# Optimization experiments

Measured on AMD Instinct MI355X. Metric: run time of the kernel, lower is better.

The kernel has to match this reference:

```python
import jax, jax.numpy as jnp
import numpy as np

SEQ, BS, H, I, E = 2048, 4, 2048, 4096, 8


def setup_inputs() -> dict:
    key = jax.random.key(0)
    ks = jax.random.split(key, 5)
    s = 0.02
    return {
        "hidden_states": jax.random.normal(ks[0], (SEQ, BS, H), dtype=jnp.float32),
        "router_w": jax.random.normal(ks[1], (H, E), dtype=jnp.float32) * s,
        "gate_w": jax.random.normal(ks[2], (E, H, I), dtype=jnp.float32) * s,
        "up_w": jax.random.normal(ks[3], (E, H, I), dtype=jnp.float32) * s,
        "down_w": jax.random.normal(ks[4], (E, I, H), dtype=jnp.float32) * s,
    }


def reference(hidden_states, router_w, gate_w, up_w, down_w):
    # Router: [S,B,H] @ [H,E] -> [S,B,E]; top-1 routing (num_experts_per_tok == 1)
    router_logits = jnp.einsum("sbh,he->sbe", hidden_states, router_w)
    routing_indices = jnp.argmax(router_logits, axis=-1)  # [S,B]
    # sigmoid routing weights are computed but NOT applied in the original combine
    routing_weights = jax.nn.sigmoid(jnp.max(router_logits, axis=-1))  # noqa: F841

    out = jnp.zeros_like(hidden_states)
    for e in range(E):  # small fixed expert count
        mask = (routing_indices == e)[..., None]  # [S,B,1]
        g = jnp.einsum("sbh,hi->sbi", hidden_states, gate_w[e])
        u = jnp.einsum("sbh,hi->sbi", hidden_states, up_w[e])
        y = jnp.einsum("sbi,ih->sbh", jax.nn.silu(g) * u, down_w[e])
        out = out + jnp.where(mask, y, jnp.zeros((), out.dtype))
    return out
```

## Files before the change

kernel.cpp:

```cpp
#include <hip/hip_runtime.h>
#include <hip/hip_bf16.h>

#define T_TOKENS 8192
#define H_DIM 2048
#define I_DIM 4096
#define E_EXP 8
#define PAD_ROWS 9216

typedef __bf16 bf16x8 __attribute__((ext_vector_type(8)));
typedef float floatx4 __attribute__((ext_vector_type(4)));
typedef unsigned short ushort8 __attribute__((ext_vector_type(8)));

__device__ __forceinline__ unsigned short f2bf(float f) {
  union { float f; unsigned int i; } c; c.f = f;
  unsigned int x = c.i;
  unsigned int r = x + 0x7fffu + ((x >> 16) & 1u);
  return (unsigned short)(r >> 16);
}

__device__ __forceinline__ float bf2float(unsigned short u) {
  union { unsigned int i; float f; } c; c.i = ((unsigned int)u) << 16;
  return c.f;
}

__device__ __forceinline__ void gload_lds16(const void* g, void* l) {
  __builtin_amdgcn_global_load_lds(
      (const __attribute__((address_space(1))) void*)g,
      (__attribute__((address_space(3))) void*)l, 16, 0, 0);
}

__global__ __launch_bounds__(256) void router_kernel(const float* __restrict__ x,
                                                     const float* __restrict__ rw,
                                                     unsigned short* __restrict__ xb,
                                                     int* __restrict__ idx,
                                                     int* __restrict__ hdr) {
  const int lane = threadIdx.x & 63;
  const int t = blockIdx.x * 4 + (threadIdx.x >> 6);
  const float* xr = x + (size_t)t * H_DIM;
  unsigned short* xbr = xb + (size_t)t * H_DIM;
  float acc[8];
#pragma unroll
  for (int e = 0; e < 8; ++e) acc[e] = 0.f;
#pragma unroll
  for (int j = 0; j < 8; ++j) {
    const int c0 = (lane + j * 64) * 4;
    floatx4 v = *(const floatx4*)(xr + c0);
    ushort4 o;
    o.x = f2bf(v[0]); o.y = f2bf(v[1]); o.z = f2bf(v[2]); o.w = f2bf(v[3]);
    *(ushort4*)(xbr + c0) = o;
#pragma unroll
    for (int cc = 0; cc < 4; ++cc) {
      const float h = v[cc];
      floatx4 r0 = *(const floatx4*)(rw + (size_t)(c0 + cc) * 8);
      floatx4 r1 = *(const floatx4*)(rw + (size_t)(c0 + cc) * 8 + 4);
#pragma unroll
      for (int e = 0; e < 4; ++e) { acc[e] += h * r0[e]; acc[e + 4] += h * r1[e]; }
    }
  }
#pragma unroll
  for (int off = 32; off > 0; off >>= 1)
#pragma unroll
    for (int e = 0; e < 8; ++e) acc[e] += __shfl_xor(acc[e], off, 64);
  if (lane == 0) {
    int best = 0; float bv = acc[0];
#pragma unroll
    for (int e = 1; e < 8; ++e) if (acc[e] > bv) { bv = acc[e]; best = e; }
    idx[t] = best;
    atomicAdd(&hdr[best], 1);
  }
}

__global__ __launch_bounds__(256) void setup_kernel(int* __restrict__ hdr,
                                                    int* __restrict__ rows) {
  if (threadIdx.x == 0) {
    int b = 0;
    for (int e = 0; e < 8; ++e) {
      hdr[16 + e] = b;
      b += ((hdr[e] + 127) >> 7) << 7;
    }
  }
  for (int i = threadIdx.x; i < PAD_ROWS; i += 256) rows[i] = -1;
}

__global__ __launch_bounds__(256) void scatter_kernel(const int* __restrict__ idx,
                                                      int* __restrict__ hdr,
                                                      int* __restrict__ rows) {
  int t = blockIdx.x * 256 + threadIdx.x;
  int e = idx[t];
  int p = atomicAdd(&hdr[8 + e], 1);
  rows[hdr[16 + e] + p] = t;
}

__global__ __launch_bounds__(256) void cvt_all_kernel(const float* __restrict__ gw,
                                                      const float* __restrict__ uw,
                                                      const float* __restrict__ dw,
                                                      unsigned short* __restrict__ Wg,
                                                      unsigned short* __restrict__ Wu,
                                                      unsigned short* __restrict__ Wd) {
  int bid = blockIdx.x;
  const float* W; unsigned short* Wt; int K, N;
  if (bid < 16384) {
    W = (bid < 8192) ? gw : uw; Wt = (bid < 8192) ? Wg : Wu;
    K = H_DIM; N = I_DIM;
    bid &= 8191;
  } else {
    W = dw; Wt = Wd; K = I_DIM; N = H_DIM;
    bid -= 16384;
  }
  const int e = bid >> 10;
  const int rem = bid & 1023;
  const int nper = N >> 10;
  const int nbx = rem & (nper - 1);
  const int kg = rem / nper;
  const int nb = nbx * 1024;
  const int n0 = threadIdx.x * 4;
  const float* src = W + (size_t)e * K * N + (size_t)kg * 8 * N + nb + n0;
  unsigned short* dst = Wt + (size_t)e * K * N
                        + ((size_t)kg * (N >> 4) + (nb >> 4)) * 128;
  floatx4 a[8];
#pragma unroll
  for (int kk = 0; kk < 8; ++kk) a[kk] = *(const floatx4*)(src + (size_t)kk * N);
#pragma unroll
  for (int nn = 0; nn < 4; ++nn) {
    const int n = n0 + nn;
    ushort8 o;
#pragma unroll
    for (int kk = 0; kk < 8; ++kk) o[kk] = f2bf(a[kk][nn]);
    *(ushort8*)(dst + (size_t)(n >> 4) * 128 + (n & 15) * 8) = o;
  }
}

__global__ __launch_bounds__(256) void cvt_gu_kernel(const float* __restrict__ gw,
                                                     const float* __restrict__ uw,
                                                     unsigned short* __restrict__ Wg,
                                                     unsigned short* __restrict__ Wu) {
  const int z = blockIdx.z;
  const int e = z & 7;
  const float* W = (z < 8) ? gw : uw;
  unsigned short* Wt = (z < 8) ? Wg : Wu;
  const int kg = blockIdx.y;
  const int nb = blockIdx.x * 1024;
  const int n0 = threadIdx.x * 4;
  const float* src = W + (size_t)e * H_DIM * I_DIM + (size_t)kg * 8 * I_DIM + nb + n0;
  unsigned short* dst = Wt + (size_t)e * H_DIM * I_DIM
                        + ((size_t)kg * (I_DIM >> 4) + (nb >> 4)) * 128;
  floatx4 a[8];
#pragma unroll
  for (int kk = 0; kk < 8; ++kk) a[kk] = *(const floatx4*)(src + (size_t)kk * I_DIM);
#pragma unroll
  for (int nn = 0; nn < 4; ++nn) {
    const int n = n0 + nn;
    ushort8 o;
#pragma unroll
    for (int kk = 0; kk < 8; ++kk) o[kk] = f2bf(a[kk][nn]);
    *(ushort8*)(dst + (size_t)(n >> 4) * 128 + (n & 15) * 8) = o;
  }
}

template <int K, int N>
__global__ __launch_bounds__(256) void cvt_tile_kernel(const float* __restrict__ W,
                                                       unsigned short* __restrict__ Wt) {
  const int e = blockIdx.z;
  const int kg = blockIdx.y;
  const int nb = blockIdx.x * 1024;
  const int n0 = threadIdx.x * 4;
  const float* src = W + (size_t)e * K * N + (size_t)kg * 8 * N + nb + n0;
  unsigned short* dst = Wt + (size_t)e * K * N
                        + ((size_t)kg * (N / 16) + (nb >> 4)) * 128;
  floatx4 a[8];
#pragma unroll
  for (int kk = 0; kk < 8; ++kk) a[kk] = *(const floatx4*)(src + (size_t)kk * N);
#pragma unroll
  for (int nn = 0; nn < 4; ++nn) {
    const int n = n0 + nn;
    ushort8 o;
#pragma unroll
    for (int kk = 0; kk < 8; ++kk) o[kk] = f2bf(a[kk][nn]);
    *(ushort8*)(dst + (size_t)(n >> 4) * 128 + (n & 15) * 8) = o;
  }
}

__global__ __launch_bounds__(256, 2) void moe_gemm_gu(
    const unsigned short* __restrict__ A,
    const unsigned short* __restrict__ Bg,
    const unsigned short* __restrict__ Bu,
    const int* __restrict__ hdr,
    const int* __restrict__ rows,
    unsigned short* __restrict__ inter) {
  const int e = blockIdx.z;
  const int cnt = hdr[e];
  if ((int)blockIdx.y * 128 >= cnt) return;
  const int seg = hdr[16 + e];

  const int tid = threadIdx.x;
  const int lane = tid & 63;
  const int wv = tid >> 6;
  const int wm = (wv & 1) * 64;
  const int wn = (wv >> 1) * 64;
  const int q = lane >> 4;
  const int l15 = lane & 15;

  __shared__ unsigned short sA[128 * 64];
  __shared__ unsigned short sBg[64 * 128];
  __shared__ unsigned short sBu[64 * 128];

  const int lr = lane >> 3;
  const int colsw = (lane & 7) ^ lr;
  const unsigned short* aptr[4];
#pragma unroll
  for (int j = 0; j < 4; ++j) {
    const int R = j * 32 + wv * 8 + lr;
    int ar = rows[seg + blockIdx.y * 128 + R];
    if (ar < 0) ar = 0;
    aptr[j] = A + (size_t)ar * H_DIM + colsw * 8;
  }

  const int N16 = I_DIM / 16;
  const int ng0 = blockIdx.x * 8;
  const unsigned short* BgE = Bg + (size_t)e * I_DIM * H_DIM;
  const unsigned short* BuE = Bu + (size_t)e * I_DIM * H_DIM;

  floatx4 accg[4][4], accu[4][4];
#pragma unroll
  for (int a = 0; a < 4; ++a)
#pragma unroll
    for (int b = 0; b < 4; ++b) {
      accg[a][b] = (floatx4){0.f, 0.f, 0.f, 0.f};
      accu[a][b] = (floatx4){0.f, 0.f, 0.f, 0.f};
    }

  const int ubB = q * 1024 + l15 * 8;
  const int wn16o = (wn >> 4) * 128;

  for (int kt = 0; kt < H_DIM; kt += 64) {
#pragma unroll
    for (int j = 0; j < 4; ++j) {
      gload_lds16(aptr[j] + kt, sA + (j * 32 + wv * 8) * 64);
      const int g = j * 4 + wv;
      const int kgg = (kt >> 3) + (g >> 1);
      const size_t so = (size_t)(kgg * N16 + ng0 + (g & 1) * 4) * 128 + lane * 8;
      gload_lds16(BgE + so, sBg + g * 512);
      gload_lds16(BuE + so, sBu + g * 512);
    }
    __syncthreads();
#pragma unroll
    for (int ks = 0; ks < 64; ks += 32) {
      const int sbase = ks >> 3;
      const int bbase = ks * 128 + wn16o + ubB;
      bf16x8 af[4], bfr[4];
#pragma unroll
      for (int fm = 0; fm < 4; ++fm) {
        const int ra = wm + fm * 16 + l15;
        af[fm] = __builtin_bit_cast(bf16x8,
            *(const ushort8*)(sA + ra * 64 + (((q + sbase) ^ (ra & 7)) << 3)));
      }
#pragma unroll
      for (int fn = 0; fn < 4; ++fn)
        bfr[fn] = __builtin_bit_cast(bf16x8,
            *(const ushort8*)(sBg + bbase + fn * 128));
#pragma unroll
      for (int fm = 0; fm < 4; ++fm)
#pragma unroll
        for (int fn = 0; fn < 4; ++fn)
          accg[fm][fn] = __builtin_amdgcn_mfma_f32_16x16x32_bf16(af[fm], bfr[fn],
                                                                 accg[fm][fn], 0, 0, 0);
#pragma unroll
      for (int fn = 0; fn < 4; ++fn)
        bfr[fn] = __builtin_bit_cast(bf16x8,
            *(const ushort8*)(sBu + bbase + fn * 128));
#pragma unroll
      for (int fm = 0; fm < 4; ++fm)
#pragma unroll
        for (int fn = 0; fn < 4; ++fn)
          accu[fm][fn] = __builtin_amdgcn_mfma_f32_16x16x32_bf16(af[fm], bfr[fn],
                                                                 accu[fm][fn], 0, 0, 0);
    }
    __syncthreads();
  }

#pragma unroll
  for (int fm = 0; fm < 4; ++fm)
#pragma unroll
    for (int fn = 0; fn < 4; ++fn)
#pragma unroll
      for (int rr = 0; rr < 4; ++rr) {
        const int row = wm + fm * 16 + q * 4 + rr;
        const int col = wn + fn * 16 + l15;
        const int gm = blockIdx.y * 128 + row;
        const int gn = blockIdx.x * 128 + col;
        const float g = accg[fm][fn][rr];
        const float u = accu[fm][fn][rr];
        const float s = g / (1.f + __expf(-g));
        inter[(size_t)(seg + gm) * I_DIM + gn] = f2bf(s * u);
      }
}

__global__ __launch_bounds__(256, 2) void moe_gemm_down(
    const unsigned short* __restrict__ A,
    const unsigned short* __restrict__ Bt,
    const int* __restrict__ hdr,
    const int* __restrict__ rows,
    float* __restrict__ outp) {
  const int e = blockIdx.z;
  const int cnt = hdr[e];
  if ((int)blockIdx.y * 128 >= cnt) return;
  const int seg = hdr[16 + e];

  const int tid = threadIdx.x;
  const int lane = tid & 63;
  const int wv = tid >> 6;
  const int wm = (wv & 1) * 64;
  const int wn = (wv >> 1) * 64;
  const int q = lane >> 4;
  const int l15 = lane & 15;

  __shared__ unsigned short sA[128 * 64];
  __shared__ unsigned short sB0[64 * 128];
  __shared__ unsigned short sB1[64 * 128];

  const int lr = lane >> 3;
  const int colsw = (lane & 7) ^ lr;
  const unsigned short* aptr[4];
#pragma unroll
  for (int j = 0; j < 4; ++j) {
    const int R = j * 32 + wv * 8 + lr;
    aptr[j] = A + (size_t)(seg + blockIdx.y * 128 + R) * I_DIM + colsw * 8;
  }

  const int N16 = H_DIM / 16;
  const int ng0 = blockIdx.x * 16;
  const unsigned short* Be = Bt + (size_t)e * H_DIM * I_DIM;

  floatx4 acc0[4][4], acc1[4][4];
#pragma unroll
  for (int a = 0; a < 4; ++a)
#pragma unroll
    for (int b = 0; b < 4; ++b) {
      acc0[a][b] = (floatx4){0.f, 0.f, 0.f, 0.f};
      acc1[a][b] = (floatx4){0.f, 0.f, 0.f, 0.f};
    }

  const int ubB = q * 1024 + l15 * 8;
  const int wn16o = (wn >> 4) * 128;

  for (int kt = 0; kt < I_DIM; kt += 64) {
#pragma unroll
    for (int j = 0; j < 4; ++j) {
      gload_lds16(aptr[j] + kt, sA + (j * 32 + wv * 8) * 64);
      const int g = j * 4 + wv;
      const int kgg = (kt >> 3) + (g >> 1);
      const size_t so0 = (size_t)(kgg * N16 + ng0 + (g & 1) * 4) * 128 + lane * 8;
      const size_t so1 = (size_t)(kgg * N16 + ng0 + 8 + (g & 1) * 4) * 128 + lane * 8;
      gload_lds16(Be + so0, sB0 + g * 512);
      gload_lds16(Be + so1, sB1 + g * 512);
    }
    __syncthreads();
#pragma unroll
    for (int ks = 0; ks < 64; ks += 32) {
      const int sbase = ks >> 3;
      const int bbase = ks * 128 + wn16o + ubB;
      bf16x8 af[4], bfr[4];
#pragma unroll
      for (int fm = 0; fm < 4; ++fm) {
        const int ra = wm + fm * 16 + l15;
        af[fm] = __builtin_bit_cast(bf16x8,
            *(const ushort8*)(sA + ra * 64 + (((q + sbase) ^ (ra & 7)) << 3)));
      }
#pragma unroll
      for (int fn = 0; fn < 4; ++fn)
        bfr[fn] = __builtin_bit_cast(bf16x8,
            *(const ushort8*)(sB0 + bbase + fn * 128));
#pragma unroll
      for (int fm = 0; fm < 4; ++fm)
#pragma unroll
        for (int fn = 0; fn < 4; ++fn)
          acc0[fm][fn] = __builtin_amdgcn_mfma_f32_16x16x32_bf16(af[fm], bfr[fn],
                                                                 acc0[fm][fn], 0, 0, 0);
#pragma unroll
      for (int fn = 0; fn < 4; ++fn)
        bfr[fn] = __builtin_bit_cast(bf16x8,
            *(const ushort8*)(sB1 + bbase + fn * 128));
#pragma unroll
      for (int fm = 0; fm < 4; ++fm)
#pragma unroll
        for (int fn = 0; fn < 4; ++fn)
          acc1[fm][fn] = __builtin_amdgcn_mfma_f32_16x16x32_bf16(af[fm], bfr[fn],
                                                                 acc1[fm][fn], 0, 0, 0);
    }
    __syncthreads();
  }

#pragma unroll
  for (int fm = 0; fm < 4; ++fm)
#pragma unroll
    for (int rr = 0; rr < 4; ++rr) {
      const int row = wm + fm * 16 + q * 4 + rr;
      const int tok = rows[seg + blockIdx.y * 128 + row];
      if (tok < 0) continue;
      float* orow = outp + (size_t)tok * H_DIM + blockIdx.x * 256;
#pragma unroll
      for (int fn = 0; fn < 4; ++fn) {
        const int col = wn + fn * 16 + l15;
        orow[col]       = acc0[fm][fn][rr];
        orow[128 + col] = acc1[fm][fn][rr];
      }
    }
}

extern "C" void kernel_launch(void* const* d_in, const int* in_sizes, int n_in,
                              void* d_out, int out_size, void* d_ws, size_t ws_size,
                              hipStream_t stream) {
  const float* hidden   = (const float*)d_in[0];
  const float* router_w = (const float*)d_in[1];
  const float* gate_w   = (const float*)d_in[2];
  const float* up_w     = (const float*)d_in[3];
  const float* down_w   = (const float*)d_in[4];
  float* out = (float*)d_out;

  char* ws = (char*)d_ws;
  int* hdr  = (int*)ws;
  int* idx  = (int*)(ws + 1024);
  int* rows = (int*)(ws + 33792);
  unsigned short* x_bf  = (unsigned short*)(ws + 70656);
  unsigned short* inter = (unsigned short*)(ws + 33625088);
  unsigned short* W1    = (unsigned short*)(ws + 109122560);
  unsigned short* W2    = (unsigned short*)(ws + 243340288);
  unsigned short* W3    = (unsigned short*)(ws + 377558016);
  const bool big = ws_size >= 511775744ull;

  hipMemsetAsync(hdr, 0, 128, stream);
  router_kernel<<<T_TOKENS / 4, 256, 0, stream>>>(hidden, router_w, x_bf, idx, hdr);
  setup_kernel<<<1, 256, 0, stream>>>(hdr, rows);
  scatter_kernel<<<T_TOKENS / 256, 256, 0, stream>>>(idx, hdr, rows);

  if (big) {
    cvt_all_kernel<<<24576, 256, 0, stream>>>(gate_w, up_w, down_w, W1, W2, W3);
    moe_gemm_gu<<<dim3(I_DIM / 128, 64, E_EXP), 256, 0, stream>>>(
        x_bf, W1, W2, hdr, rows, inter);
    moe_gemm_down<<<dim3(H_DIM / 256, 64, E_EXP), 256, 0, stream>>>(
        inter, W3, hdr, rows, out);
  } else {
    cvt_gu_kernel<<<dim3(4, 256, 16), 256, 0, stream>>>(gate_w, up_w, W1, W2);
    moe_gemm_gu<<<dim3(I_DIM / 128, 64, E_EXP), 256, 0, stream>>>(
        x_bf, W1, W2, hdr, rows, inter);
    cvt_tile_kernel<I_DIM, H_DIM><<<dim3(2, 512, 8), 256, 0, stream>>>(down_w, W1);
    moe_gemm_down<<<dim3(H_DIM / 256, 64, E_EXP), 256, 0, stream>>>(
        inter, W1, hdr, rows, out);
  }
}
```

Measured before the change: 1.469 ms.

## Double-buffer MoE GEMM LDS tiles with BK=32, k-major A layout, and priority hints

```diff
diff --git a/kernel.cpp b/kernel.cpp
--- a/kernel.cpp
+++ b/kernel.cpp
@@ -119,7 +119,8 @@
                         + ((size_t)kg * (N >> 4) + (nb >> 4)) * 128;
   floatx4 a[8];
 #pragma unroll
-  for (int kk = 0; kk < 8; ++kk) a[kk] = *(const floatx4*)(src + (size_t)kk * N);
+  for (int kk = 0; kk < 8; ++kk)
+    a[kk] = __builtin_nontemporal_load((const floatx4*)(src + (size_t)kk * N));
 #pragma unroll
   for (int nn = 0; nn < 4; ++nn) {
     const int n = n0 + nn;
@@ -146,7 +147,8 @@
                         + ((size_t)kg * (I_DIM >> 4) + (nb >> 4)) * 128;
   floatx4 a[8];
 #pragma unroll
-  for (int kk = 0; kk < 8; ++kk) a[kk] = *(const floatx4*)(src + (size_t)kk * I_DIM);
+  for (int kk = 0; kk < 8; ++kk)
+    a[kk] = __builtin_nontemporal_load((const floatx4*)(src + (size_t)kk * I_DIM));
 #pragma unroll
   for (int nn = 0; nn < 4; ++nn) {
     const int n = n0 + nn;
@@ -169,7 +171,8 @@
                         + ((size_t)kg * (N / 16) + (nb >> 4)) * 128;
   floatx4 a[8];
 #pragma unroll
-  for (int kk = 0; kk < 8; ++kk) a[kk] = *(const floatx4*)(src + (size_t)kk * N);
+  for (int kk = 0; kk < 8; ++kk)
+    a[kk] = __builtin_nontemporal_load((const floatx4*)(src + (size_t)kk * N));
 #pragma unroll
   for (int nn = 0; nn < 4; ++nn) {
     const int n = n0 + nn;
@@ -180,7 +183,7 @@
   }
 }
 
-__global__ __launch_bounds__(256, 2) void moe_gemm_gu(
+__global__ __launch_bounds__(256, 3) void moe_gemm_gu(
     const unsigned short* __restrict__ A,
     const unsigned short* __restrict__ Bg,
     const unsigned short* __restrict__ Bu,
@@ -200,20 +203,17 @@
   const int q = lane >> 4;
   const int l15 = lane & 15;
 
-  __shared__ unsigned short sA[128 * 64];
-  __shared__ unsigned short sBg[64 * 128];
-  __shared__ unsigned short sBu[64 * 128];
-
-  const int lr = lane >> 3;
-  const int colsw = (lane & 7) ^ lr;
-  const unsigned short* aptr[4];
-#pragma unroll
-  for (int j = 0; j < 4; ++j) {
-    const int R = j * 32 + wv * 8 + lr;
-    int ar = rows[seg + blockIdx.y * 128 + R];
-    if (ar < 0) ar = 0;
-    aptr[j] = A + (size_t)ar * H_DIM + colsw * 8;
-  }
+  __shared__ unsigned short sA[2][4096];
+  __shared__ unsigned short sBg[2][4096];
+  __shared__ unsigned short sBu[2][4096];
+
+  const int Rst = (wv & 1) * 64 + lane;
+  int ar = rows[seg + blockIdx.y * 128 + Rst];
+  if (ar < 0) ar = 0;
+  const unsigned short* aA = A + (size_t)ar * H_DIM;
+  const int s0 = wv >> 1;
+  const int dA0 = wv * 512;
+  const int dA1 = (wv + 4) * 512;
 
   const int N16 = I_DIM / 16;
   const int ng0 = blockIdx.x * 8;
@@ -229,54 +229,65 @@
       accu[a][b] = (floatx4){0.f, 0.f, 0.f, 0.f};
     }
 
-  const int ubB = q * 1024 + l15 * 8;
-  const int wn16o = (wn >> 4) * 128;
-
-  for (int kt = 0; kt < H_DIM; kt += 64) {
-#pragma unroll
-    for (int j = 0; j < 4; ++j) {
-      gload_lds16(aptr[j] + kt, sA + (j * 32 + wv * 8) * 64);
-      const int g = j * 4 + wv;
-      const int kgg = (kt >> 3) + (g >> 1);
-      const size_t so = (size_t)(kgg * N16 + ng0 + (g & 1) * 4) * 128 + lane * 8;
-      gload_lds16(BgE + so, sBg + g * 512);
-      gload_lds16(BuE + so, sBu + g * 512);
-    }
-    __syncthreads();
-#pragma unroll
-    for (int ks = 0; ks < 64; ks += 32) {
-      const int sbase = ks >> 3;
-      const int bbase = ks * 128 + wn16o + ubB;
-      bf16x8 af[4], bfr[4];
-#pragma unroll
-      for (int fm = 0; fm < 4; ++fm) {
-        const int ra = wm + fm * 16 + l15;
-        af[fm] = __builtin_bit_cast(bf16x8,
-            *(const ushort8*)(sA + ra * 64 + (((q + sbase) ^ (ra & 7)) << 3)));
-      }
+  const int wn16 = wn >> 4;
+
+#define STAGE_GU(buf, kt)                                                      \
+  do {                                                                         \
+    gload_lds16(aA + (kt) + s0 * 8, &sA[buf][dA0]);                            \
+    gload_lds16(aA + (kt) + (s0 + 2) * 8, &sA[buf][dA1]);                      \
+    const size_t bo = ((size_t)(((kt) >> 3) + wv) * N16 + ng0) * 128 + lane * 8;\
+    gload_lds16(BgE + bo, &sBg[buf][wv * 1024]);                               \
+    gload_lds16(BgE + bo + 512, &sBg[buf][wv * 1024 + 512]);                   \
+    gload_lds16(BuE + bo, &sBu[buf][wv * 1024]);                               \
+    gload_lds16(BuE + bo + 512, &sBu[buf][wv * 1024 + 512]);                   \
+  } while (0)
+
+  STAGE_GU(0, 0);
+  for (int t = 0; t < 64; ++t) {
+    if (t < 63) {
+      STAGE_GU((t + 1) & 1, (t + 1) * 32);
+      asm volatile("s_waitcnt vmcnt(6)" ::: "memory");
+    } else {
+      asm volatile("s_waitcnt vmcnt(0)" ::: "memory");
+    }
+    __builtin_amdgcn_sched_barrier(0);
+    __builtin_amdgcn_s_barrier();
+    const unsigned short* sAc = sA[t & 1];
+    const unsigned short* sBgc = sBg[t & 1];
+    const unsigned short* sBuc = sBu[t & 1];
+    bf16x8 af[4], bfr[4];
+#pragma unroll
+    for (int fm = 0; fm < 4; ++fm)
+      af[fm] = __builtin_bit_cast(bf16x8,
+          *(const ushort8*)(sAc + q * 1024 + (wm + fm * 16 + l15) * 8));
+#pragma unroll
+    for (int fn = 0; fn < 4; ++fn)
+      bfr[fn] = __builtin_bit_cast(bf16x8,
+          *(const ushort8*)(sBgc + (q * 8 + wn16 + fn) * 128 + l15 * 8));
+    __builtin_amdgcn_s_setprio(1);
+#pragma unroll
+    for (int fm = 0; fm < 4; ++fm)
 #pragma unroll
       for (int fn = 0; fn < 4; ++fn)
-        bfr[fn] = __builtin_bit_cast(bf16x8,
-            *(const ushort8*)(sBg + bbase + fn * 128));
-#pragma unroll
-      for (int fm = 0; fm < 4; ++fm)
-#pragma unroll
-        for (int fn = 0; fn < 4; ++fn)
-          accg[fm][fn] = __builtin_amdgcn_mfma_f32_16x16x32_bf16(af[fm], bfr[fn],
-                                                                 accg[fm][fn], 0, 0, 0);
+        accg[fm][fn] = __builtin_amdgcn_mfma_f32_16x16x32_bf16(af[fm], bfr[fn],
+                                                               accg[fm][fn], 0, 0, 0);
+    __builtin_amdgcn_s_setprio(0);
+#pragma unroll
+    for (int fn = 0; fn < 4; ++fn)
+      bfr[fn] = __builtin_bit_cast(bf16x8,
+          *(const ushort8*)(sBuc + (q * 8 + wn16 + fn) * 128 + l15 * 8));
+    __builtin_amdgcn_s_setprio(1);
+#pragma unroll
+    for (int fm = 0; fm < 4; ++fm)
 #pragma unroll
       for (int fn = 0; fn < 4; ++fn)
-        bfr[fn] = __builtin_bit_cast(bf16x8,
-            *(const ushort8*)(sBu + bbase + fn * 128));
-#pragma unroll
-      for (int fm = 0; fm < 4; ++fm)
-#pragma unroll
-        for (int fn = 0; fn < 4; ++fn)
-          accu[fm][fn] = __builtin_amdgcn_mfma_f32_16x16x32_bf16(af[fm], bfr[fn],
-                                                                 accu[fm][fn], 0, 0, 0);
-    }
-    __syncthreads();
-  }
+        accu[fm][fn] = __builtin_amdgcn_mfma_f32_16x16x32_bf16(af[fm], bfr[fn],
+                                                               accu[fm][fn], 0, 0, 0);
+    __builtin_amdgcn_s_setprio(0);
+    __builtin_amdgcn_sched_barrier(0);
+    __builtin_amdgcn_s_barrier();
+  }
+#undef STAGE_GU
 
 #pragma unroll
   for (int fm = 0; fm < 4; ++fm)
@@ -295,7 +306,7 @@
       }
 }
 
-__global__ __launch_bounds__(256, 2) void moe_gemm_down(
+__global__ __launch_bounds__(256, 3) void moe_gemm_down(
     const unsigned short* __restrict__ A,
     const unsigned short* __restrict__ Bt,
     const int* __restrict__ hdr,
@@ -314,18 +325,15 @@
   const int q = lane >> 4;
   const int l15 = lane & 15;
 
-  __shared__ unsigned short sA[128 * 64];
-  __shared__ unsigned short sB0[64 * 128];
-  __shared__ unsigned short sB1[64 * 128];
-
-  const int lr = lane >> 3;
-  const int colsw = (lane & 7) ^ lr;
-  const unsigned short* aptr[4];
-#pragma unroll
-  for (int j = 0; j < 4; ++j) {
-    const int R = j * 32 + wv * 8 + lr;
-    aptr[j] = A + (size_t)(seg + blockIdx.y * 128 + R) * I_DIM + colsw * 8;
-  }
+  __shared__ unsigned short sA[2][4096];
+  __shared__ unsigned short sB0[2][4096];
+  __shared__ unsigned short sB1[2][4096];
+
+  const int Rst = (wv & 1) * 64 + lane;
+  const unsigned short* aA = A + (size_t)(seg + blockIdx.y * 128 + Rst) * I_DIM;
+  const int s0 = wv >> 1;
+  const int dA0 = wv * 512;
+  const int dA1 = (wv + 4) * 512;
 
   const int N16 = H_DIM / 16;
   const int ng0 = blockIdx.x * 16;
@@ -340,55 +348,65 @@
       acc1[a][b] = (floatx4){0.f, 0.f, 0.f, 0.f};
     }
 
-  const int ubB = q * 1024 + l15 * 8;
-  const int wn16o = (wn >> 4) * 128;
-
-  for (int kt = 0; kt < I_DIM; kt += 64) {
-#pragma unroll
-    for (int j = 0; j < 4; ++j) {
-      gload_lds16(aptr[j] + kt, sA + (j * 32 + wv * 8) * 64);
-      const int g = j * 4 + wv;
-      const int kgg = (kt >> 3) + (g >> 1);
-      const size_t so0 = (size_t)(kgg * N16 + ng0 + (g & 1) * 4) * 128 + lane * 8;
-      const size_t so1 = (size_t)(kgg * N16 + ng0 + 8 + (g & 1) * 4) * 128 + lane * 8;
-      gload_lds16(Be + so0, sB0 + g * 512);
-      gload_lds16(Be + so1, sB1 + g * 512);
-    }
-    __syncthreads();
-#pragma unroll
-    for (int ks = 0; ks < 64; ks += 32) {
-      const int sbase = ks >> 3;
-      const int bbase = ks * 128 + wn16o + ubB;
-      bf16x8 af[4], bfr[4];
-#pragma unroll
-      for (int fm = 0; fm < 4; ++fm) {
-        const int ra = wm + fm * 16 + l15;
-        af[fm] = __builtin_bit_cast(bf16x8,
-            *(const ushort8*)(sA + ra * 64 + (((q + sbase) ^ (ra & 7)) << 3)));
-      }
+  const int wn16 = wn >> 4;
+
+#define STAGE_DN(buf, kt)                                                      \
+  do {                                                                         \
+    gload_lds16(aA + (kt) + s0 * 8, &sA[buf][dA0]);                            \
+    gload_lds16(aA + (kt) + (s0 + 2) * 8, &sA[buf][dA1]);                      \
+    const size_t bo = ((size_t)(((kt) >> 3) + wv) * N16 + ng0) * 128 + lane * 8;\
+    gload_lds16(Be + bo, &sB0[buf][wv * 1024]);                                \
+    gload_lds16(Be + bo + 512, &sB0[buf][wv * 1024 + 512]);                    \
+    gload_lds16(Be + bo + 1024, &sB1[buf][wv * 1024]);                         \
+    gload_lds16(Be + bo + 1536, &sB1[buf][wv * 1024 + 512]);                   \
+  } while (0)
+
+  STAGE_DN(0, 0);
+  for (int t = 0; t < 128; ++t) {
+    if (t < 127) {
+      STAGE_DN((t + 1) & 1, (t + 1) * 32);
+      asm volatile("s_waitcnt vmcnt(6)" ::: "memory");
+    } else {
+      asm volatile("s_waitcnt vmcnt(0)" ::: "memory");
+    }
+    __builtin_amdgcn_sched_barrier(0);
+    __builtin_amdgcn_s_barrier();
+    const unsigned short* sAc = sA[t & 1];
+    const unsigned short* sB0c = sB0[t & 1];
+    const unsigned short* sB1c = sB1[t & 1];
+    bf16x8 af[4], bfr[4];
+#pragma unroll
+    for (int fm = 0; fm < 4; ++fm)
+      af[fm] = __builtin_bit_cast(bf16x8,
+          *(const ushort8*)(sAc + q * 1024 + (wm + fm * 16 + l15) * 8));
+#pragma unroll
+    for (int fn = 0; fn < 4; ++fn)
+      bfr[fn] = __builtin_bit_cast(bf16x8,
+          *(const ushort8*)(sB0c + (q * 8 + wn16 + fn) * 128 + l15 * 8));
+    __builtin_amdgcn_s_setprio(1);
+#pragma unroll
+    for (int fm = 0; fm < 4; ++fm)
 #pragma unroll
       for (int fn = 0; fn < 4; ++fn)
-        bfr[fn] = __builtin_bit_cast(bf16x8,
-            *(const ushort8*)(sB0 + bbase + fn * 128));
-#pragma unroll
-      for (int fm = 0; fm < 4; ++fm)
-#pragma unroll
-        for (int fn = 0; fn < 4; ++fn)
-          acc0[fm][fn] = __builtin_amdgcn_mfma_f32_16x16x32_bf16(af[fm], bfr[fn],
-                                                                 acc0[fm][fn], 0, 0, 0);
+        acc0[fm][fn] = __builtin_amdgcn_mfma_f32_16x16x32_bf16(af[fm], bfr[fn],
+                                                               acc0[fm][fn], 0, 0, 0);
+    __builtin_amdgcn_s_setprio(0);
+#pragma unroll
+    for (int fn = 0; fn < 4; ++fn)
+      bfr[fn] = __builtin_bit_cast(bf16x8,
+          *(const ushort8*)(sB1c + (q * 8 + wn16 + fn) * 128 + l15 * 8));
+    __builtin_amdgcn_s_setprio(1);
+#pragma unroll
+    for (int fm = 0; fm < 4; ++fm)
 #pragma unroll
       for (int fn = 0; fn < 4; ++fn)
-        bfr[fn] = __builtin_bit_cast(bf16x8,
-            *(const ushort8*)(sB1 + bbase + fn * 128));
-#pragma unroll
-      for (int fm = 0; fm < 4; ++fm)
-#pragma unroll
-        for (int fn = 0; fn < 4; ++fn)
-          acc1[fm][fn] = __builtin_amdgcn_mfma_f32_16x16x32_bf16(af[fm], bfr[fn],
-                                                                 acc1[fm][fn], 0, 0, 0);
-    }
-    __syncthreads();
-  }
+        acc1[fm][fn] = __builtin_amdgcn_mfma_f32_16x16x32_bf16(af[fm], bfr[fn],
+                                                               acc1[fm][fn], 0, 0, 0);
+    __builtin_amdgcn_s_setprio(0);
+    __builtin_amdgcn_sched_barrier(0);
+    __builtin_amdgcn_s_barrier();
+  }
+#undef STAGE_DN
 
 #pragma unroll
   for (int fm = 0; fm < 4; ++fm)
```

After: 1.628 ms. +10.8%, slower.
